# Performance work log

Measured on AMD Instinct MI355X. Metric: run time of the kernel, lower is better.

## Reference

```python
import jax, jax.numpy as jnp
import numpy as np

TYPE_PANEL, TYPE_DIALOG, TYPE_CHAR = 1, 2, 3
NUM_ELEMS = 64  # max element index per type (panel count cap per page)
B, S, D = 8, 4096, 768
NPC, NDS = 4, 4  # num_panel_classes, num_dialog_shapes


def setup_inputs() -> dict:
    key = jax.random.key(0)
    ks = jax.random.split(key, 16)
    w = lambda k, shp: jax.random.normal(k, shp, dtype=jnp.float32) * 0.02
    return {
        "element_types": jax.random.randint(ks[0], (B, S), 0, 4, dtype=jnp.int32),
        "element_indices": jax.random.randint(ks[1], (B, S), 0, NUM_ELEMS, dtype=jnp.int32),
        "parent_panel_indices": jax.random.randint(ks[2], (B, S), 0, NUM_ELEMS, dtype=jnp.int32),
        "style_vector": jax.random.normal(ks[3], (B, 4), dtype=jnp.float32),
        "type_emb": w(ks[4], (4, D)),
        "index_emb": w(ks[5], (NUM_ELEMS, D)),
        "parent_emb": w(ks[6], (NUM_ELEMS, D)),
        "style_w": w(ks[7], (4, D)),
        "style_b": jnp.zeros((D,), jnp.float32),
        "ln_g": jnp.ones((D,), jnp.float32),
        "ln_b": jnp.zeros((D,), jnp.float32),
        "panel_w": w(ks[8], (D, NPC + 4)),
        "panel_b": jnp.zeros((NPC + 4,), jnp.float32),
        "dialog_w": w(ks[9], (2 * D, NDS + 4)),
        "dialog_b": jnp.zeros((NDS + 4,), jnp.float32),
        "char_w": w(ks[10], (2 * D, 4)),
        "char_b": jnp.zeros((4,), jnp.float32),
    }


def reference(element_types, element_indices, parent_panel_indices, style_vector,
              type_emb, index_emb, parent_emb, style_w, style_b, ln_g, ln_b,
              panel_w, panel_b, dialog_w, dialog_b, char_w, char_b):
    Bv, Sv = element_types.shape
    # --- TokenLayoutEncoder: embedding sum + style projection + LayerNorm ---
    x = type_emb[element_types] + index_emb[element_indices] + parent_emb[parent_panel_indices]
    x = x + (style_vector @ style_w + style_b)[:, None, :]
    mu = x.mean(-1, keepdims=True)
    var = ((x - mu) ** 2).mean(-1, keepdims=True)
    feats = (x - mu) * jax.lax.rsqrt(var + 1e-5) * ln_g + ln_b  # (B,S,D)

    # --- vectorized _build_parent_remap: orig panel idx -> kept panel order pos ---
    panel_mask = element_types == TYPE_PANEL                      # (B,S)
    kept = (jnp.cumsum(panel_mask, axis=1) - 1).astype(jnp.int32) # order pos of each panel token
    brow = jnp.arange(Bv, dtype=jnp.int32)[:, None]
    col = jnp.where(panel_mask, element_indices, NUM_ELEMS)       # dummy slot for non-panels
    remap = (jnp.full((Bv, NUM_ELEMS + 1), -1, jnp.int32)
             .at[brow, col].max(kept))[:, :NUM_ELEMS]             # (B, NUM_ELEMS)
    # kept panel order pos -> sequence position (for parent feature gather)
    slot = jnp.where(panel_mask, kept, Sv)
    seq_ids = jnp.broadcast_to(jnp.arange(Sv, dtype=jnp.int32), (Bv, Sv))
    pos_table = (jnp.zeros((Bv, Sv + 1), jnp.int32)
                 .at[brow, slot].set(seq_ids))[:, :Sv]            # (B,S)

    # --- parent_pos per token (DIALOG/CHAR only), -1 otherwise ---
    child_mask = (element_types == TYPE_DIALOG) | (element_types == TYPE_CHAR)
    ppos = jnp.where(child_mask,
                     jnp.take_along_axis(remap, parent_panel_indices, axis=1), -1)
    valid = ppos >= 0
    pseq = jnp.take_along_axis(pos_table, jnp.clip(ppos, 0, Sv - 1), axis=1)
    parent_feats = jnp.take_along_axis(feats, pseq[..., None], axis=1)
    parent_feats = parent_feats * valid[..., None].astype(feats.dtype)
    cat = jnp.concatenate([feats, parent_feats], axis=-1)         # (B,S,2D)

    # --- ParallelPredictionHeads, masked per token type ---
    panel_out = (feats @ panel_w + panel_b) * panel_mask[..., None].astype(feats.dtype)
    dmask = ((element_types == TYPE_DIALOG) & valid)[..., None].astype(feats.dtype)
    cmask = ((element_types == TYPE_CHAR) & valid)[..., None].astype(feats.dtype)
    dialog_out = (cat @ dialog_w + dialog_b) * dmask
    char_out = (cat @ char_w + char_b) * cmask
    return panel_out, dialog_out, char_out
```

## Files before the change

### kernel.cpp

```cpp
#include <hip/hip_runtime.h>

#define NB 8
#define NS 4096
#define ND 768

#define WPACK_F4 6528
#define LDS_F4   6720

typedef float4 f4;

static __device__ __forceinline__ f4 ld4(const float* __restrict__ p, int i) {
    return ((const f4*)p)[i];
}

static __device__ __forceinline__ void dot4(float& acc, const f4& a, const f4& w) {
    acc = fmaf(a.x, w.x, acc);
    acc = fmaf(a.y, w.y, acc);
    acc = fmaf(a.z, w.z, acc);
    acc = fmaf(a.w, w.w, acc);
}

__global__ __launch_bounds__(256) void lp_pre(
    const int* __restrict__ et, const int* __restrict__ ei,
    const float* __restrict__ sv, const float* __restrict__ sw,
    const float* __restrict__ sb,
    const float* __restrict__ pw, const float* __restrict__ dw,
    const float* __restrict__ cw,
    const float* __restrict__ lng, const float* __restrict__ lnb,
    int* __restrict__ table, float* __restrict__ sprj,
    float* __restrict__ wpack)
{
    const int bx = blockIdx.x;
    if (bx < 128) {
        int t = bx * 256 + threadIdx.x;
        if (et[t] == 1) {
            int b = t >> 12;
            atomicMax(&table[b * 64 + ei[t]], t & (NS - 1));
        }
    } else if (bx < 130) {
        const int lane = threadIdx.x & 63;
        const int b = (bx - 128) * 4 + (threadIdx.x >> 6);
        const float sv0 = sv[b*4+0], sv1 = sv[b*4+1], sv2 = sv[b*4+2], sv3 = sv[b*4+3];
        #pragma unroll
        for (int g = 0; g < 3; ++g) {
            int i = g*64 + lane;
            f4 w0 = ld4(sw, i), w1 = ld4(sw, 192+i), w2 = ld4(sw, 384+i), w3 = ld4(sw, 576+i);
            f4 bb = ld4(sb, i);
            f4 r;
            r.x = bb.x + sv0*w0.x + sv1*w1.x + sv2*w2.x + sv3*w3.x;
            r.y = bb.y + sv0*w0.y + sv1*w1.y + sv2*w2.y + sv3*w3.y;
            r.z = bb.z + sv0*w0.z + sv1*w1.z + sv2*w2.z + sv3*w3.z;
            r.w = bb.w + sv0*w0.w + sv1*w1.w + sv2*w2.w + sv3*w3.w;
            ((f4*)(sprj + b*ND))[i] = r;
        }
    } else {
        const int q = (bx - 130) * 256 + threadIdx.x;
        if (q >= WPACK_F4) return;
        f4 r;
        if (q < 1536) {
            int o = q / 192, i = q - o * 192, d0 = 4 * i;
            r.x = pw[(d0+0)*8 + o];
            r.y = pw[(d0+1)*8 + o];
            r.z = pw[(d0+2)*8 + o];
            r.w = pw[(d0+3)*8 + o];
        } else if (q < 4608) {
            int u = q - 1536;
            int o = u / 384, i = u - o * 384;
            int d0 = (i < 192) ? 4*i : 768 + 4*(i - 192);
            r.x = dw[(d0+0)*8 + o];
            r.y = dw[(d0+1)*8 + o];
            r.z = dw[(d0+2)*8 + o];
            r.w = dw[(d0+3)*8 + o];
        } else if (q < 6144) {
            int u = q - 4608;
            int o = u / 384, i = u - o * 384;
            int d0 = (i < 192) ? 4*i : 768 + 4*(i - 192);
            r.x = cw[(d0+0)*4 + o];
            r.y = cw[(d0+1)*4 + o];
            r.z = cw[(d0+2)*4 + o];
            r.w = cw[(d0+3)*4 + o];
        } else if (q < 6336) {
            r = ld4(lng, q - 6144);
        } else {
            r = ld4(lnb, q - 6336);
        }
        ((f4*)wpack)[q] = r;
    }
}

__global__ __launch_bounds__(256) void lp_parent(
    const int* __restrict__ ei, const int* __restrict__ ppi,
    const float* __restrict__ temb, const float* __restrict__ iemb,
    const float* __restrict__ pemb, const float* __restrict__ lng,
    const float* __restrict__ lnb,
    const int* __restrict__ table, const float* __restrict__ sprj,
    float* __restrict__ pfeat)
{
    const int lane = threadIdx.x & 63;
    const int slot = blockIdx.x * 4 + (threadIdx.x >> 6);
    const int b = slot >> 6;
    const int pp = table[slot];
    if (pp < 0) return;
    const int ptok = b * NS + pp;
    const int pei = ei[ptok], pppi = ppi[ptok];
    const float* ie = iemb + pei * ND;
    const float* pe = pemb + pppi * ND;
    const float* sp = sprj + b * ND;

    f4 x[3]; float s1 = 0.f, sq = 0.f;
    #pragma unroll
    for (int g = 0; g < 3; ++g) {
        int i = g*64 + lane;
        f4 a = ld4(temb + ND, i), c = ld4(ie, i), d = ld4(pe, i), s = ld4(sp, i);
        f4 v;
        v.x = a.x + c.x + d.x + s.x;
        v.y = a.y + c.y + d.y + s.y;
        v.z = a.z + c.z + d.z + s.z;
        v.w = a.w + c.w + d.w + s.w;
        x[g] = v;
        s1 += v.x + v.y + v.z + v.w;
        sq = fmaf(v.x, v.x, sq);
        sq = fmaf(v.y, v.y, sq);
        sq = fmaf(v.z, v.z, sq);
        sq = fmaf(v.w, v.w, sq);
    }
    #pragma unroll
    for (int k = 32; k >= 1; k >>= 1) {
        s1 += __shfl_xor(s1, k, 64);
        sq += __shfl_xor(sq, k, 64);
    }
    float mu = s1 * (1.f/ND);
    float rs = rsqrtf(sq * (1.f/ND) - mu * mu + 1e-5f);
    float c0 = -mu * rs;
    float* dst = pfeat + (size_t)slot * ND;
    #pragma unroll
    for (int g = 0; g < 3; ++g) {
        int i = g*64 + lane;
        f4 gg = ld4(lng, i), bb = ld4(lnb, i);
        f4 v = x[g], xn;
        xn.x = fmaf(v.x, rs, c0); v.x = fmaf(xn.x, gg.x, bb.x);
        xn.y = fmaf(v.y, rs, c0); v.y = fmaf(xn.y, gg.y, bb.y);
        xn.z = fmaf(v.z, rs, c0); v.z = fmaf(xn.z, gg.z, bb.z);
        xn.w = fmaf(v.w, rs, c0); v.w = fmaf(xn.w, gg.w, bb.w);
        ((f4*)dst)[i] = v;
    }
}

__global__ __launch_bounds__(1024) void lp_main(
    const int* __restrict__ et, const int* __restrict__ ei, const int* __restrict__ ppi,
    const float* __restrict__ temb, const float* __restrict__ iemb,
    const float* __restrict__ pemb,
    const float* __restrict__ pb, const float* __restrict__ db,
    const float* __restrict__ cb,
    const int* __restrict__ table, const float* __restrict__ sprj,
    const float* __restrict__ wpack, const float* __restrict__ pfeat,
    float* __restrict__ out)
{
    __shared__ f4 S[LDS_F4];
    const int tid = threadIdx.x;
    const int lane = tid & 63;
    const int wid = tid >> 6;
    const int bx = blockIdx.x;
    const int b = bx >> 5;

    for (int i = tid; i < WPACK_F4; i += 1024) S[i] = ((const f4*)wpack)[i];
    if (tid < 192) S[WPACK_F4 + tid] = ((const f4*)(sprj + b * ND))[tid];
    __syncthreads();

    int t = bx * 128 + wid;
    int type = et[t], my_ei = ei[t], my_ppi = ppi[t];

    for (int r = 0; r < 8; ++r) {
        const int tn = t + 16;
        int type_n = 0, ei_n = 0, ppi_n = 0;
        if (r < 7) { type_n = et[tn]; ei_n = ei[tn]; ppi_n = ppi[tn]; }

        f4 z4; z4.x = 0.f; z4.y = 0.f; z4.z = 0.f; z4.w = 0.f;
        f4 po0 = z4, po1 = z4, dq0 = z4, dq1 = z4, cq0 = z4;

        if (type != 0) {
            int pp = -1;
            if (type != 1) pp = table[b * 64 + my_ppi];

            const float* te = temb + type * ND;
            const float* ie = iemb + my_ei * ND;
            const float* pe = pemb + my_ppi * ND;

            f4 x[3];
            float s1 = 0.f, sq = 0.f;
            #pragma unroll
            for (int g = 0; g < 3; ++g) {
                int i = g * 64 + lane;
                f4 a = ld4(te, i), c = ld4(ie, i), d = ld4(pe, i);
                f4 s = S[WPACK_F4 + i];
                f4 v;
                v.x = a.x + c.x + d.x + s.x;
                v.y = a.y + c.y + d.y + s.y;
                v.z = a.z + c.z + d.z + s.z;
                v.w = a.w + c.w + d.w + s.w;
                x[g] = v;
                s1 += v.x + v.y + v.z + v.w;
                sq = fmaf(v.x, v.x, sq);
                sq = fmaf(v.y, v.y, sq);
                sq = fmaf(v.z, v.z, sq);
                sq = fmaf(v.w, v.w, sq);
            }
            #pragma unroll
            for (int k = 32; k >= 1; k >>= 1) {
                s1 += __shfl_xor(s1, k, 64);
                sq += __shfl_xor(sq, k, 64);
            }
            float mu = s1 * (1.f / ND);
            float rs = rsqrtf(sq * (1.f / ND) - mu * mu + 1e-5f);
            float c0 = -mu * rs;
            #pragma unroll
            for (int g = 0; g < 3; ++g) {
                int i = g * 64 + lane;
                f4 gg = S[6144 + i], bb = S[6336 + i];
                f4 v = x[g], xn;
                xn.x = fmaf(v.x, rs, c0); v.x = fmaf(xn.x, gg.x, bb.x);
                xn.y = fmaf(v.y, rs, c0); v.y = fmaf(xn.y, gg.y, bb.y);
                xn.z = fmaf(v.z, rs, c0); v.z = fmaf(xn.z, gg.z, bb.z);
                xn.w = fmaf(v.w, rs, c0); v.w = fmaf(xn.w, gg.w, bb.w);
                x[g] = v;
            }

            if (type == 1) {
                float acc[8];
                #pragma unroll
                for (int o = 0; o < 8; ++o) acc[o] = 0.f;
                #pragma unroll
                for (int g = 0; g < 3; ++g) {
                    int i = g * 64 + lane;
                    #pragma unroll
                    for (int o = 0; o < 8; ++o)
                        dot4(acc[o], x[g], S[o * 192 + i]);
                }
                #pragma unroll
                for (int k = 32; k >= 1; k >>= 1) {
                    #pragma unroll
                    for (int o = 0; o < 8; ++o)
                        acc[o] += __shfl_xor(acc[o], k, 64);
                }
                po0.x = acc[0] + pb[0]; po0.y = acc[1] + pb[1];
                po0.z = acc[2] + pb[2]; po0.w = acc[3] + pb[3];
                po1.x = acc[4] + pb[4]; po1.y = acc[5] + pb[5];
                po1.z = acc[6] + pb[6]; po1.w = acc[7] + pb[7];
            } else if (pp >= 0) {
                const float* pfr = pfeat + (size_t)(b * 64 + my_ppi) * ND;
                if (type == 2) {
                    float acc[8];
                    #pragma unroll
                    for (int o = 0; o < 8; ++o) acc[o] = 0.f;
                    #pragma unroll
                    for (int g = 0; g < 3; ++g) {
                        int i = g * 64 + lane;
                        #pragma unroll
                        for (int o = 0; o < 8; ++o)
                            dot4(acc[o], x[g], S[1536 + o * 384 + i]);
                    }
                    #pragma unroll
                    for (int g = 0; g < 3; ++g)
                        x[g] = ld4(pfr, g * 64 + lane);
                    #pragma unroll
                    for (int g = 0; g < 3; ++g) {
                        int i = g * 64 + lane;
                        #pragma unroll
                        for (int o = 0; o < 8; ++o)
                            dot4(acc[o], x[g], S[1536 + o * 384 + 192 + i]);
                    }
                    #pragma unroll
                    for (int k = 32; k >= 1; k >>= 1) {
                        #pragma unroll
                        for (int o = 0; o < 8; ++o)
                            acc[o] += __shfl_xor(acc[o], k, 64);
                    }
                    dq0.x = acc[0] + db[0]; dq0.y = acc[1] + db[1];
                    dq0.z = acc[2] + db[2]; dq0.w = acc[3] + db[3];
                    dq1.x = acc[4] + db[4]; dq1.y = acc[5] + db[5];
                    dq1.z = acc[6] + db[6]; dq1.w = acc[7] + db[7];
                } else {
                    float acc[4];
                    #pragma unroll
                    for (int o = 0; o < 4; ++o) acc[o] = 0.f;
                    #pragma unroll
                    for (int g = 0; g < 3; ++g) {
                        int i = g * 64 + lane;
                        #pragma unroll
                        for (int o = 0; o < 4; ++o)
                            dot4(acc[o], x[g], S[4608 + o * 384 + i]);
                    }
                    #pragma unroll
                    for (int g = 0; g < 3; ++g)
                        x[g] = ld4(pfr, g * 64 + lane);
                    #pragma unroll
                    for (int g = 0; g < 3; ++g) {
                        int i = g * 64 + lane;
                        #pragma unroll
                        for (int o = 0; o < 4; ++o)
                            dot4(acc[o], x[g], S[4608 + o * 384 + 192 + i]);
                    }
                    #pragma unroll
                    for (int k = 32; k >= 1; k >>= 1) {
                        #pragma unroll
                        for (int o = 0; o < 4; ++o)
                            acc[o] += __shfl_xor(acc[o], k, 64);
                    }
                    cq0.x = acc[0] + cb[0]; cq0.y = acc[1] + cb[1];
                    cq0.z = acc[2] + cb[2]; cq0.w = acc[3] + cb[3];
                }
            }
        }

        if (lane == 0) {
            f4* op = (f4*)(out + (size_t)t * 8);
            op[0] = po0; op[1] = po1;
            f4* od = (f4*)(out + (size_t)NB * NS * 8 + (size_t)t * 8);
            od[0] = dq0; od[1] = dq1;
            ((f4*)(out + (size_t)NB * NS * 16 + (size_t)t * 4))[0] = cq0;
        }

        t = tn; type = type_n; my_ei = ei_n; my_ppi = ppi_n;
    }
}

extern "C" void kernel_launch(void* const* d_in, const int* in_sizes, int n_in,
                              void* d_out, int out_size, void* d_ws, size_t ws_size,
                              hipStream_t stream) {
    const int* et  = (const int*)d_in[0];
    const int* ei  = (const int*)d_in[1];
    const int* ppi = (const int*)d_in[2];
    const float* sv   = (const float*)d_in[3];
    const float* temb = (const float*)d_in[4];
    const float* iemb = (const float*)d_in[5];
    const float* pemb = (const float*)d_in[6];
    const float* sw   = (const float*)d_in[7];
    const float* sb   = (const float*)d_in[8];
    const float* lng  = (const float*)d_in[9];
    const float* lnb  = (const float*)d_in[10];
    const float* pw   = (const float*)d_in[11];
    const float* pb   = (const float*)d_in[12];
    const float* dw   = (const float*)d_in[13];
    const float* db   = (const float*)d_in[14];
    const float* cw   = (const float*)d_in[15];
    const float* cbp  = (const float*)d_in[16];
    float* out = (float*)d_out;

    int*   table = (int*)d_ws;
    float* sprj  = (float*)((char*)d_ws + 4096);
    float* wpack = (float*)((char*)d_ws + 32768);
    float* pfeat = (float*)((char*)d_ws + 32768 + WPACK_F4 * 16);

    hipMemsetAsync(table, 0xFF, NB * 64 * sizeof(int), stream);

    lp_pre<<<156, 256, 0, stream>>>(et, ei, sv, sw, sb, pw, dw, cw, lng, lnb,
                                    table, sprj, wpack);
    lp_parent<<<128, 256, 0, stream>>>(ei, ppi, temb, iemb, pemb, lng, lnb,
                                       table, sprj, pfeat);
    lp_main<<<256, 1024, 0, stream>>>(et, ei, ppi, temb, iemb, pemb,
                                      pb, db, cbp,
                                      table, sprj, wpack, pfeat, out);
}
```

Baseline: 130.6 us.

## Fuse setup kernels into one launch with LDS panel table and prefetch parent features

Merges the memset, preprocessing kernel and parent-feature LayerNorm kernel into a single 16-block setup kernel. Each batch block builds its panel table with shared-memory atomics and computes the parent features in place. In the main kernel the parent feature row is loaded before the LayerNorm reduction, and the two halves of each dot product are interleaved to hide global-load latency. This removes two launches and a memset, at the cost of far fewer blocks doing the setup work and higher register pressure in the main kernel.

Measured after the change: 138.8 us. 1.06x slower.

```diff
diff --git a/kernel.cpp b/kernel.cpp
--- a/kernel.cpp
+++ b/kernel.cpp
@@ -20,27 +20,40 @@
     acc = fmaf(a.w, w.w, acc);
 }
 
-__global__ __launch_bounds__(256) void lp_pre(
-    const int* __restrict__ et, const int* __restrict__ ei,
+__global__ __launch_bounds__(1024) void lp_setup(
+    const int* __restrict__ et, const int* __restrict__ ei, const int* __restrict__ ppi,
     const float* __restrict__ sv, const float* __restrict__ sw,
     const float* __restrict__ sb,
+    const float* __restrict__ temb, const float* __restrict__ iemb,
+    const float* __restrict__ pemb,
+    const float* __restrict__ lng, const float* __restrict__ lnb,
     const float* __restrict__ pw, const float* __restrict__ dw,
     const float* __restrict__ cw,
-    const float* __restrict__ lng, const float* __restrict__ lnb,
     int* __restrict__ table, float* __restrict__ sprj,
-    float* __restrict__ wpack)
+    float* __restrict__ wpack, float* __restrict__ pfeat)
 {
     const int bx = blockIdx.x;
-    if (bx < 128) {
-        int t = bx * 256 + threadIdx.x;
-        if (et[t] == 1) {
-            int b = t >> 12;
-            atomicMax(&table[b * 64 + ei[t]], t & (NS - 1));
-        }
-    } else if (bx < 130) {
-        const int lane = threadIdx.x & 63;
-        const int b = (bx - 128) * 4 + (threadIdx.x >> 6);
-        const float sv0 = sv[b*4+0], sv1 = sv[b*4+1], sv2 = sv[b*4+2], sv3 = sv[b*4+3];
+    const int tid = threadIdx.x;
+
+    if (bx < NB) {
+        __shared__ int ltab[64];
+        const int lane = tid & 63;
+        const int wid = tid >> 6;
+        if (tid < 64) ltab[tid] = -1;
+        __syncthreads();
+
+        const int base = bx * NS;
+        #pragma unroll
+        for (int r = 0; r < 4; ++r) {
+            int s = r * 1024 + tid;
+            int tok = base + s;
+            if (et[tok] == 1) atomicMax(&ltab[ei[tok]], s);
+        }
+        __syncthreads();
+        if (tid < 64) table[bx * 64 + tid] = ltab[tid];
+
+        const float sv0 = sv[bx*4+0], sv1 = sv[bx*4+1], sv2 = sv[bx*4+2], sv3 = sv[bx*4+3];
+        f4 sp[3];
         #pragma unroll
         for (int g = 0; g < 3; ++g) {
             int i = g*64 + lane;
@@ -51,10 +64,59 @@
             r.y = bb.y + sv0*w0.y + sv1*w1.y + sv2*w2.y + sv3*w3.y;
             r.z = bb.z + sv0*w0.z + sv1*w1.z + sv2*w2.z + sv3*w3.z;
             r.w = bb.w + sv0*w0.w + sv1*w1.w + sv2*w2.w + sv3*w3.w;
-            ((f4*)(sprj + b*ND))[i] = r;
+            sp[g] = r;
+            if (wid == 0) ((f4*)(sprj + bx*ND))[i] = r;
+        }
+
+        for (int r = 0; r < 4; ++r) {
+            const int slot = r * 16 + wid;
+            const int pp = ltab[slot];
+            if (pp < 0) continue;
+            const int ptok = base + pp;
+            const int pei = ei[ptok], pppi = ppi[ptok];
+            const float* ie = iemb + pei * ND;
+            const float* pe = pemb + pppi * ND;
+
+            f4 x[3]; float s1 = 0.f, sq = 0.f;
+            #pragma unroll
+            for (int g = 0; g < 3; ++g) {
+                int i = g*64 + lane;
+                f4 a = ld4(temb + ND, i), c = ld4(ie, i), d = ld4(pe, i);
+                f4 v;
+                v.x = a.x + c.x + d.x + sp[g].x;
+                v.y = a.y + c.y + d.y + sp[g].y;
+                v.z = a.z + c.z + d.z + sp[g].z;
+                v.w = a.w + c.w + d.w + sp[g].w;
+                x[g] = v;
+                s1 += v.x + v.y + v.z + v.w;
+                sq = fmaf(v.x, v.x, sq);
+                sq = fmaf(v.y, v.y, sq);
+                sq = fmaf(v.z, v.z, sq);
+                sq = fmaf(v.w, v.w, sq);
+            }
+            #pragma unroll
+            for (int k = 32; k >= 1; k >>= 1) {
+                s1 += __shfl_xor(s1, k, 64);
+                sq += __shfl_xor(sq, k, 64);
+            }
+            float mu = s1 * (1.f/ND);
+            float rs = rsqrtf(sq * (1.f/ND) - mu * mu + 1e-5f);
+            float c0 = -mu * rs;
+            float* dst = pfeat + (size_t)(bx * 64 + slot) * ND;
+            #pragma unroll
+            for (int g = 0; g < 3; ++g) {
+                int i = g*64 + lane;
+                f4 gg = ld4(lng, i), bb = ld4(lnb, i);
+                f4 v = x[g], xn;
+                xn.x = fmaf(v.x, rs, c0); v.x = fmaf(xn.x, gg.x, bb.x);
+                xn.y = fmaf(v.y, rs, c0); v.y = fmaf(xn.y, gg.y, bb.y);
+                xn.z = fmaf(v.z, rs, c0); v.z = fmaf(xn.z, gg.z, bb.z);
+                xn.w = fmaf(v.w, rs, c0); v.w = fmaf(xn.w, gg.w, bb.w);
+                ((f4*)dst)[i] = v;
+            }
         }
     } else {
-        const int q = (bx - 130) * 256 + threadIdx.x;
+        const int q = (bx - NB) * 1024 + tid;
         if (q >= WPACK_F4) return;
         f4 r;
         if (q < 1536) {
@@ -88,64 +150,6 @@
     }
 }
 
-__global__ __launch_bounds__(256) void lp_parent(
-    const int* __restrict__ ei, const int* __restrict__ ppi,
-    const float* __restrict__ temb, const float* __restrict__ iemb,
-    const float* __restrict__ pemb, const float* __restrict__ lng,
-    const float* __restrict__ lnb,
-    const int* __restrict__ table, const float* __restrict__ sprj,
-    float* __restrict__ pfeat)
-{
-    const int lane = threadIdx.x & 63;
-    const int slot = blockIdx.x * 4 + (threadIdx.x >> 6);
-    const int b = slot >> 6;
-    const int pp = table[slot];
-    if (pp < 0) return;
-    const int ptok = b * NS + pp;
-    const int pei = ei[ptok], pppi = ppi[ptok];
-    const float* ie = iemb + pei * ND;
-    const float* pe = pemb + pppi * ND;
-    const float* sp = sprj + b * ND;
-
-    f4 x[3]; float s1 = 0.f, sq = 0.f;
-    #pragma unroll
-    for (int g = 0; g < 3; ++g) {
-        int i = g*64 + lane;
-        f4 a = ld4(temb + ND, i), c = ld4(ie, i), d = ld4(pe, i), s = ld4(sp, i);
-        f4 v;
-        v.x = a.x + c.x + d.x + s.x;
-        v.y = a.y + c.y + d.y + s.y;
-        v.z = a.z + c.z + d.z + s.z;
-        v.w = a.w + c.w + d.w + s.w;
-        x[g] = v;
-        s1 += v.x + v.y + v.z + v.w;
-        sq = fmaf(v.x, v.x, sq);
-        sq = fmaf(v.y, v.y, sq);
-        sq = fmaf(v.z, v.z, sq);
-        sq = fmaf(v.w, v.w, sq);
-    }
-    #pragma unroll
-    for (int k = 32; k >= 1; k >>= 1) {
-        s1 += __shfl_xor(s1, k, 64);
-        sq += __shfl_xor(sq, k, 64);
-    }
-    float mu = s1 * (1.f/ND);
-    float rs = rsqrtf(sq * (1.f/ND) - mu * mu + 1e-5f);
-    float c0 = -mu * rs;
-    float* dst = pfeat + (size_t)slot * ND;
-    #pragma unroll
-    for (int g = 0; g < 3; ++g) {
-        int i = g*64 + lane;
-        f4 gg = ld4(lng, i), bb = ld4(lnb, i);
-        f4 v = x[g], xn;
-        xn.x = fmaf(v.x, rs, c0); v.x = fmaf(xn.x, gg.x, bb.x);
-        xn.y = fmaf(v.y, rs, c0); v.y = fmaf(xn.y, gg.y, bb.y);
-        xn.z = fmaf(v.z, rs, c0); v.z = fmaf(xn.z, gg.z, bb.z);
-        xn.w = fmaf(v.w, rs, c0); v.w = fmaf(xn.w, gg.w, bb.w);
-        ((f4*)dst)[i] = v;
-    }
-}
-
 __global__ __launch_bounds__(1024) void lp_main(
     const int* __restrict__ et, const int* __restrict__ ei, const int* __restrict__ ppi,
     const float* __restrict__ temb, const float* __restrict__ iemb,
@@ -205,6 +209,16 @@
                 sq = fmaf(v.z, v.z, sq);
                 sq = fmaf(v.w, v.w, sq);
             }
+
+            f4 xp[3];
+            const bool child = (type != 1) && (pp >= 0);
+            if (child) {
+                const float* pfr = pfeat + (size_t)(b * 64 + my_ppi) * ND;
+                #pragma unroll
+                for (int g = 0; g < 3; ++g)
+                    xp[g] = ld4(pfr, g * 64 + lane);
+            }
+
             #pragma unroll
             for (int k = 32; k >= 1; k >>= 1) {
                 s1 += __shfl_xor(s1, k, 64);
@@ -246,8 +260,7 @@
                 po0.z = acc[2] + pb[2]; po0.w = acc[3] + pb[3];
                 po1.x = acc[4] + pb[4]; po1.y = acc[5] + pb[5];
                 po1.z = acc[6] + pb[6]; po1.w = acc[7] + pb[7];
-            } else if (pp >= 0) {
-                const float* pfr = pfeat + (size_t)(b * 64 + my_ppi) * ND;
+            } else if (child) {
                 if (type == 2) {
                     float acc[8];
                     #pragma unroll
@@ -256,18 +269,10 @@
                     for (int g = 0; g < 3; ++g) {
                         int i = g * 64 + lane;
                         #pragma unroll
-                        for (int o = 0; o < 8; ++o)
-                            dot4(acc[o], x[g], S[1536 + o * 384 + i]);
-                    }
-                    #pragma unroll
-                    for (int g = 0; g < 3; ++g)
-                        x[g] = ld4(pfr, g * 64 + lane);
-                    #pragma unroll
-                    for (int g = 0; g < 3; ++g) {
-                        int i = g * 64 + lane;
-                        #pragma unroll
-                        for (int o = 0; o < 8; ++o)
-                            dot4(acc[o], x[g], S[1536 + o * 384 + 192 + i]);
+                        for (int o = 0; o < 8; ++o) {
+                            dot4(acc[o], x[g],  S[1536 + o * 384 + i]);
+                            dot4(acc[o], xp[g], S[1536 + o * 384 + 192 + i]);
+                        }
                     }
                     #pragma unroll
                     for (int k = 32; k >= 1; k >>= 1) {
@@ -287,18 +292,10 @@
                     for (int g = 0; g < 3; ++g) {
                         int i = g * 64 + lane;
                         #pragma unroll
-                        for (int o = 0; o < 4; ++o)
-                            dot4(acc[o], x[g], S[4608 + o * 384 + i]);
-                    }
-                    #pragma unroll
-                    for (int g = 0; g < 3; ++g)
-                        x[g] = ld4(pfr, g * 64 + lane);
-                    #pragma unroll
-                    for (int g = 0; g < 3; ++g) {
-                        int i = g * 64 + lane;
-                        #pragma unroll
-                        for (int o = 0; o < 4; ++o)
-                            dot4(acc[o], x[g], S[4608 + o * 384 + 192 + i]);
+                        for (int o = 0; o < 4; ++o) {
+                            dot4(acc[o], x[g],  S[4608 + o * 384 + i]);
+                            dot4(acc[o], xp[g], S[4608 + o * 384 + 192 + i]);
+                        }
                     }
                     #pragma unroll
                     for (int k = 32; k >= 1; k >>= 1) {
@@ -351,12 +348,9 @@
     float* wpack = (float*)((char*)d_ws + 32768);
     float* pfeat = (float*)((char*)d_ws + 32768 + WPACK_F4 * 16);
 
-    hipMemsetAsync(table, 0xFF, NB * 64 * sizeof(int), stream);
-
-    lp_pre<<<156, 256, 0, stream>>>(et, ei, sv, sw, sb, pw, dw, cw, lng, lnb,
-                                    table, sprj, wpack);
-    lp_parent<<<128, 256, 0, stream>>>(ei, ppi, temb, iemb, pemb, lng, lnb,
-                                       table, sprj, pfeat);
+    lp_setup<<<16, 1024, 0, stream>>>(et, ei, ppi, sv, sw, sb, temb, iemb, pemb,
+                                      lng, lnb, pw, dw, cw,
+                                      table, sprj, wpack, pfeat);
     lp_main<<<256, 1024, 0, stream>>>(et, ei, ppi, temb, iemb, pemb,
                                       pb, db, cbp,
                                       table, sprj, wpack, pfeat, out);
```
